# Optimization experiments

Hardware: AMD Instinct MI355X
Metric: run time of the kernel (lower is better)

Reference implementation:

```python
import jax, jax.numpy as jnp
import numpy as np

F_KERNEL = 3
STD = 0.25


def _dense_grid(w):
    # w: (B,2,H,W) flow. Returns normalized sampling coords gx, gy in [-1,1],
    # grid = identity_grid - flow (emited/flow DenseGridGen semantics).
    B, _, H, W = w.shape
    base_x = jnp.linspace(-1.0, 1.0, W, dtype=w.dtype)[None, None, :]   # (1,1,W)
    base_y = jnp.linspace(-1.0, 1.0, H, dtype=w.dtype)[None, :, None]   # (1,H,1)
    gx = base_x - w[:, 0]   # (B,H,W)
    gy = base_y - w[:, 1]   # (B,H,W)
    return gx, gy


def _gaussian_grid_sample(im, gx, gy, F=F_KERNEL, std=STD):
    # im: (B,C,H,W); gx, gy: (B,Ho,Wo) normalized coords (align_corners=True).
    # For each output pixel gather an FxF neighborhood around floor(pixel coord)
    # and accumulate with unnormalized Gaussian weights; zeros padding.
    B, C, H, W = im.shape
    x = (gx + 1.0) * 0.5 * (W - 1)   # pixel-space x
    y = (gy + 1.0) * 0.5 * (H - 1)   # pixel-space y
    ix = jnp.floor(x).astype(jnp.int32)
    iy = jnp.floor(y).astype(jnp.int32)
    inv2s2 = 1.0 / (2.0 * std * std)
    flat = im.reshape(B, C, H * W)
    Ho, Wo = gx.shape[1], gx.shape[2]
    out = jnp.zeros((B, C, Ho, Wo), dtype=im.dtype)
    half = F // 2
    for dy in range(F):
        for dx in range(F):
            xi = ix + (dx - half)   # (B,Ho,Wo) tap column index
            yi = iy + (dy - half)   # tap row index
            wgt = jnp.exp(-((x - xi) ** 2 + (y - yi) ** 2) * inv2s2)
            valid = (xi >= 0) & (xi < W) & (yi >= 0) & (yi < H)
            xc = jnp.clip(xi, 0, W - 1)
            yc = jnp.clip(yi, 0, H - 1)
            idx = (yc * W + xc).reshape(B, 1, Ho * Wo)
            v = jnp.take_along_axis(flat, jnp.broadcast_to(idx, (B, C, Ho * Wo)), axis=2)
            v = v.reshape(B, C, Ho, Wo)
            out = out + (wgt * valid.astype(im.dtype))[:, None] * v
    return out


def setup_inputs() -> dict:
    key = jax.random.key(0)
    k1, k2 = jax.random.split(key)
    im = jax.random.normal(k1, (8, 16, 256, 256), dtype=jnp.float32)
    w = jax.random.normal(k2, (8, 2, 256, 256), dtype=jnp.float32) * 0.1
    return {"im": im, "w": w}


def reference(im, w):
    gx, gy = _dense_grid(w)
    return _gaussian_grid_sample(im, gx, gy)
```

## Files before the change

kernel.cpp:

```cpp
#include <hip/hip_runtime.h>

constexpr int B = 8, C = 16, H = 256, W = 256;
constexpr float INV2S2 = 8.0f;
constexpr int HW = H * W;
constexpr int NXCD = 8;

__global__ __launch_bounds__(256) void transpose_nchw_nhwc(
    const float* __restrict__ im, float* __restrict__ nhwc) {
  const int vblk = (blockIdx.x & (NXCD - 1)) * (2048 / NXCD) + (blockIdx.x >> 3);
  const int idx = vblk * 256 + threadIdx.x;
  const int b = idx >> 16;
  const int pix = idx & (HW - 1);
  const float* __restrict__ src = im + (size_t)b * C * HW + pix;
  float v[C];
#pragma unroll
  for (int c = 0; c < C; ++c) v[c] = __builtin_nontemporal_load(src + (size_t)c * HW);
  float4* __restrict__ dst = (float4*)(nhwc + (size_t)idx * C);
#pragma unroll
  for (int q = 0; q < 4; ++q)
    dst[q] = make_float4(v[4 * q], v[4 * q + 1], v[4 * q + 2], v[4 * q + 3]);
}

__global__ __launch_bounds__(256) void gauss_warp_nhwc(
    const float* __restrict__ nhwc, const float* __restrict__ w,
    float* __restrict__ out) {
  const int vblk = (blockIdx.x & (NXCD - 1)) * (8192 / NXCD) + (blockIdx.x >> 3);
  const int t = vblk * 256 + threadIdx.x;
  const int cq  = t & 3;
  const int idx = t >> 2;
  const int wo = idx & (W - 1);
  const int ho = (idx >> 8) & (H - 1);
  const int b  = idx >> 16;
  const int pix = ho * W + wo;

  const float w0 = w[(size_t)(b * 2 + 0) * HW + pix];
  const float w1 = w[(size_t)(b * 2 + 1) * HW + pix];

  const float x = (float)wo - w0 * (0.5f * (float)(W - 1));
  const float y = (float)ho - w1 * (0.5f * (float)(H - 1));
  const int ix = (int)floorf(x);
  const int iy = (int)floorf(y);

  float wx[3], wy[3];
  int xc[3], yc[3];
#pragma unroll
  for (int d = 0; d < 3; ++d) {
    const int xi = ix + d - 1;
    const float dx = x - (float)xi;
    wx[d] = (xi >= 0 && xi < W) ? __expf(-dx * dx * INV2S2) : 0.0f;
    xc[d] = min(max(xi, 0), W - 1);
    const int yi = iy + d - 1;
    const float dy = y - (float)yi;
    wy[d] = (yi >= 0 && yi < H) ? __expf(-dy * dy * INV2S2) : 0.0f;
    yc[d] = min(max(yi, 0), H - 1);
  }

  const float* __restrict__ base = nhwc + ((size_t)b * HW) * C + cq * 4;
  float4 acc = make_float4(0.f, 0.f, 0.f, 0.f);
#pragma unroll
  for (int dy = 0; dy < 3; ++dy) {
#pragma unroll
    for (int dx = 0; dx < 3; ++dx) {
      const float g = wy[dy] * wx[dx];
      const int off = yc[dy] * W + xc[dx];
      const float4 v = *(const float4*)(base + (size_t)off * C);
      acc.x = fmaf(g, v.x, acc.x);
      acc.y = fmaf(g, v.y, acc.y);
      acc.z = fmaf(g, v.z, acc.z);
      acc.w = fmaf(g, v.w, acc.w);
    }
  }

  float* __restrict__ ob = out + (size_t)b * C * HW + (size_t)(cq * 4) * HW + pix;
  __builtin_nontemporal_store(acc.x, ob);
  __builtin_nontemporal_store(acc.y, ob + (size_t)HW);
  __builtin_nontemporal_store(acc.z, ob + (size_t)2 * HW);
  __builtin_nontemporal_store(acc.w, ob + (size_t)3 * HW);
}

__global__ __launch_bounds__(256) void gauss_warp_kernel(
    const float* __restrict__ im, const float* __restrict__ w,
    float* __restrict__ out) {
  const int idx = blockIdx.x * 256 + threadIdx.x;
  const int wo = idx & (W - 1);
  const int ho = (idx >> 8) & (H - 1);
  const int b  = idx >> 16;
  const int pix = ho * W + wo;
  const float w0 = w[(size_t)(b * 2 + 0) * HW + pix];
  const float w1 = w[(size_t)(b * 2 + 1) * HW + pix];
  const float x = (float)wo - w0 * (0.5f * (float)(W - 1));
  const float y = (float)ho - w1 * (0.5f * (float)(H - 1));
  const int ix = (int)floorf(x);
  const int iy = (int)floorf(y);
  float wx[3], wy[3];
  int xc[3], yc[3];
#pragma unroll
  for (int d = 0; d < 3; ++d) {
    const int xi = ix + d - 1;
    const float dx = x - (float)xi;
    wx[d] = (xi >= 0 && xi < W) ? __expf(-dx * dx * INV2S2) : 0.0f;
    xc[d] = min(max(xi, 0), W - 1);
    const int yi = iy + d - 1;
    const float dy = y - (float)yi;
    wy[d] = (yi >= 0 && yi < H) ? __expf(-dy * dy * INV2S2) : 0.0f;
    yc[d] = min(max(yi, 0), H - 1);
  }
  float wgt[9];
  int off[9];
#pragma unroll
  for (int dy = 0; dy < 3; ++dy)
#pragma unroll
    for (int dx = 0; dx < 3; ++dx) {
      wgt[dy * 3 + dx] = wy[dy] * wx[dx];
      off[dy * 3 + dx] = yc[dy] * W + xc[dx];
    }
  const float* __restrict__ imb = im + (size_t)b * C * HW;
  float* __restrict__ ob = out + (size_t)b * C * HW + pix;
#pragma unroll 4
  for (int c = 0; c < C; ++c) {
    const float* __restrict__ p = imb + (size_t)c * HW;
    float acc = 0.0f;
#pragma unroll
    for (int t = 0; t < 9; ++t) acc = fmaf(wgt[t], p[off[t]], acc);
    ob[(size_t)c * HW] = acc;
  }
}

extern "C" void kernel_launch(void* const* d_in, const int* in_sizes, int n_in,
                              void* d_out, int out_size, void* d_ws, size_t ws_size,
                              hipStream_t stream) {
  const float* im = (const float*)d_in[0];
  const float* w  = (const float*)d_in[1];
  float* out = (float*)d_out;

  const size_t need = (size_t)B * C * HW * sizeof(float);
  if (ws_size >= need) {
    float* nhwc = (float*)d_ws;
    const int px = B * H * W;
    transpose_nchw_nhwc<<<px / 256, 256, 0, stream>>>(im, nhwc);
    gauss_warp_nhwc<<<px * 4 / 256, 256, 0, stream>>>(nhwc, w, out);
  } else {
    const int total = B * H * W;
    gauss_warp_kernel<<<total / 256, 256, 0, stream>>>(im, w, out);
  }
}
```

Before: 116.6 us.

## Precompute packed Gaussian tap weights in prep kernel for lean warp pass

The transpose kernel now also computes the nine Gaussian tap weights and a base linear offset once per pixel, and writes them to a 48-byte packed workspace record. The warp kernel reads this record instead of recomputing exps and clamped indices in each of its four channel-quad threads, and it clamps a single linear offset. The aim is to remove the redundant per-thread weight math. The cost is roughly 50 MB of extra global write and read traffic, and a larger workspace requirement that falls back to the slow path if the workspace is too small.

```diff
diff --git a/kernel.cpp b/kernel.cpp
--- a/kernel.cpp
+++ b/kernel.cpp
@@ -5,12 +5,15 @@
 constexpr int HW = H * W;
 constexpr int NXCD = 8;
 
-__global__ __launch_bounds__(256) void transpose_nchw_nhwc(
-    const float* __restrict__ im, float* __restrict__ nhwc) {
+
+__global__ __launch_bounds__(256) void prep_nhwc_weights(
+    const float* __restrict__ im, const float* __restrict__ w,
+    float* __restrict__ nhwc, float* __restrict__ wpack) {
   const int vblk = (blockIdx.x & (NXCD - 1)) * (2048 / NXCD) + (blockIdx.x >> 3);
   const int idx = vblk * 256 + threadIdx.x;
   const int b = idx >> 16;
   const int pix = idx & (HW - 1);
+
   const float* __restrict__ src = im + (size_t)b * C * HW + pix;
   float v[C];
 #pragma unroll
@@ -19,55 +22,65 @@
 #pragma unroll
   for (int q = 0; q < 4; ++q)
     dst[q] = make_float4(v[4 * q], v[4 * q + 1], v[4 * q + 2], v[4 * q + 3]);
-}
 
-__global__ __launch_bounds__(256) void gauss_warp_nhwc(
-    const float* __restrict__ nhwc, const float* __restrict__ w,
-    float* __restrict__ out) {
-  const int vblk = (blockIdx.x & (NXCD - 1)) * (8192 / NXCD) + (blockIdx.x >> 3);
-  const int t = vblk * 256 + threadIdx.x;
-  const int cq  = t & 3;
-  const int idx = t >> 2;
-  const int wo = idx & (W - 1);
-  const int ho = (idx >> 8) & (H - 1);
-  const int b  = idx >> 16;
-  const int pix = ho * W + wo;
-
+  const int wo = pix & (W - 1);
+  const int ho = pix >> 8;
   const float w0 = w[(size_t)(b * 2 + 0) * HW + pix];
   const float w1 = w[(size_t)(b * 2 + 1) * HW + pix];
-
   const float x = (float)wo - w0 * (0.5f * (float)(W - 1));
   const float y = (float)ho - w1 * (0.5f * (float)(H - 1));
   const int ix = (int)floorf(x);
   const int iy = (int)floorf(y);
 
   float wx[3], wy[3];
-  int xc[3], yc[3];
 #pragma unroll
   for (int d = 0; d < 3; ++d) {
     const int xi = ix + d - 1;
     const float dx = x - (float)xi;
     wx[d] = (xi >= 0 && xi < W) ? __expf(-dx * dx * INV2S2) : 0.0f;
-    xc[d] = min(max(xi, 0), W - 1);
     const int yi = iy + d - 1;
     const float dy = y - (float)yi;
     wy[d] = (yi >= 0 && yi < H) ? __expf(-dy * dy * INV2S2) : 0.0f;
-    yc[d] = min(max(yi, 0), H - 1);
   }
 
-  const float* __restrict__ base = nhwc + ((size_t)b * HW) * C + cq * 4;
+  const int base = (iy - 1) * W + (ix - 1);
+  float4* __restrict__ wp = (float4*)(wpack + (size_t)idx * 12);
+  wp[0] = make_float4(wy[0] * wx[0], wy[0] * wx[1], wy[0] * wx[2], wy[1] * wx[0]);
+  wp[1] = make_float4(wy[1] * wx[1], wy[1] * wx[2], wy[2] * wx[0], wy[2] * wx[1]);
+  wp[2] = make_float4(wy[2] * wx[2], __int_as_float(base), 0.0f, 0.0f);
+}
+
+__global__ __launch_bounds__(256) void gauss_warp_lean(
+    const float* __restrict__ nhwc, const float* __restrict__ wpack,
+    float* __restrict__ out) {
+  const int vblk = (blockIdx.x & (NXCD - 1)) * (8192 / NXCD) + (blockIdx.x >> 3);
+  const int t = vblk * 256 + threadIdx.x;
+  const int cq  = t & 3;
+  const int idx = t >> 2;
+  const int b   = idx >> 16;
+  const int pix = idx & (HW - 1);
+
+  const float4* __restrict__ wp = (const float4*)(wpack + (size_t)idx * 12);
+  const float4 p0 = wp[0];
+  const float4 p1 = wp[1];
+  const float4 p2 = wp[2];
+  const float g[9] = {p0.x, p0.y, p0.z, p0.w, p1.x, p1.y, p1.z, p1.w, p2.x};
+  const int base = __float_as_int(p2.y);
+
+  const float* __restrict__ bimg = nhwc + ((size_t)b * HW) * C + cq * 4;
   float4 acc = make_float4(0.f, 0.f, 0.f, 0.f);
 #pragma unroll
   for (int dy = 0; dy < 3; ++dy) {
 #pragma unroll
     for (int dx = 0; dx < 3; ++dx) {
-      const float g = wy[dy] * wx[dx];
-      const int off = yc[dy] * W + xc[dx];
-      const float4 v = *(const float4*)(base + (size_t)off * C);
-      acc.x = fmaf(g, v.x, acc.x);
-      acc.y = fmaf(g, v.y, acc.y);
-      acc.z = fmaf(g, v.z, acc.z);
-      acc.w = fmaf(g, v.w, acc.w);
+      int off = base + dy * W + dx;
+      off = min(max(off, 0), HW - 1);
+      const float4 vv = *(const float4*)(bimg + (size_t)off * C);
+      const float gg = g[dy * 3 + dx];
+      acc.x = fmaf(gg, vv.x, acc.x);
+      acc.y = fmaf(gg, vv.y, acc.y);
+      acc.z = fmaf(gg, vv.z, acc.z);
+      acc.w = fmaf(gg, vv.w, acc.w);
     }
   }
 
@@ -133,12 +146,14 @@
   const float* w  = (const float*)d_in[1];
   float* out = (float*)d_out;
 
-  const size_t need = (size_t)B * C * HW * sizeof(float);
-  if (ws_size >= need) {
-    float* nhwc = (float*)d_ws;
+  const size_t nhwc_bytes  = (size_t)B * HW * C * sizeof(float);
+  const size_t wpack_bytes = (size_t)B * HW * 12 * sizeof(float);
+  if (ws_size >= nhwc_bytes + wpack_bytes) {
+    float* nhwc  = (float*)d_ws;
+    float* wpack = (float*)((char*)d_ws + nhwc_bytes);
     const int px = B * H * W;
-    transpose_nchw_nhwc<<<px / 256, 256, 0, stream>>>(im, nhwc);
-    gauss_warp_nhwc<<<px * 4 / 256, 256, 0, stream>>>(nhwc, w, out);
+    prep_nhwc_weights<<<px / 256, 256, 0, stream>>>(im, w, nhwc, wpack);
+    gauss_warp_lean<<<px * 4 / 256, 256, 0, stream>>>(nhwc, wpack, out);
   } else {
     const int total = B * H * W;
     gauss_warp_kernel<<<total / 256, 256, 0, stream>>>(im, w, out);
```

New measurement: 123.1 us. 5.6% more time.
